# Kernel tuning notes

Measured on AMD Instinct MI355X. Metric: run time of the kernel, lower is better.

The kernel has to match this reference:

```python
import jax, jax.numpy as jnp
import numpy as np

D_MODEL, D_HEAD, N_HEAD, PERIOD = 1024, 64, 16, 30
B, T1, T2 = 2, 2048, 2048


def setup_inputs() -> dict:
    key = jax.random.key(0)
    ks = jax.random.split(key, 7)
    s_in = 1.0 / np.sqrt(D_MODEL)
    s_out = 1.0 / np.sqrt(N_HEAD * D_HEAD)
    return {
        "x": jax.random.normal(ks[0], (B, T1, D_MODEL), dtype=jnp.float32),
        "context": jax.random.normal(ks[1], (B, T2, D_MODEL), dtype=jnp.float32),
        "Wq": jax.random.uniform(ks[2], (N_HEAD * D_HEAD, D_MODEL), jnp.float32, -s_in, s_in),
        "Wk": jax.random.uniform(ks[3], (N_HEAD * D_HEAD, D_MODEL), jnp.float32, -s_in, s_in),
        "Wv": jax.random.uniform(ks[4], (N_HEAD * D_HEAD, D_MODEL), jnp.float32, -s_in, s_in),
        "Wo": jax.random.uniform(ks[5], (D_MODEL, N_HEAD * D_HEAD), jnp.float32, -s_out, s_out),
        "bo": jax.random.uniform(ks[6], (D_MODEL,), jnp.float32, -s_out, s_out),
    }


def reference(x, context, Wq, Wk, Wv, Wo, bo):
    Bx, T1x, _ = x.shape
    T2x = context.shape[1]
    scale = 1.0 / np.sqrt(D_HEAD).astype(np.float32)
    # projections (torch Linear: y = x @ W^T)
    q = (x @ Wq.T).reshape(Bx, T1x, N_HEAD, D_HEAD)
    k = (context @ Wk.T).reshape(Bx, T2x, N_HEAD, D_HEAD)
    v = (context @ Wv.T).reshape(Bx, T2x, N_HEAD, D_HEAD)
    # attention scores [B, H, T1, T2]
    scores = jnp.einsum('bihd,bjhd->bhij', q, k) * scale
    # ALiBi-style periodic distance bias
    dist = jnp.abs(jnp.arange(T1x)[:, None] - jnp.arange(T2x)[None, :])  # [T1,T2]
    bias = -(dist // PERIOD).astype(jnp.float32)                          # [T1,T2]
    head_scale = jnp.power(2.0, -jnp.arange(1, N_HEAD + 1, dtype=jnp.float32))
    biased = scores + bias[None, None, :, :] * head_scale[None, :, None, None]
    attn = jax.nn.softmax(biased, axis=-1)
    out = jnp.einsum('bhij,bjhd->bihd', attn, v).reshape(Bx, T1x, N_HEAD * D_HEAD)
    # output projection; dropout is identity in eval mode
    return out @ Wo.T + bo
```

## Files before the change

### kernel.cpp

```cpp
#include <hip/hip_runtime.h>
#include <hip/hip_fp16.h>

typedef _Float16 f16;
typedef __attribute__((ext_vector_type(8))) _Float16 f16x8;
typedef __attribute__((ext_vector_type(4))) _Float16 f16x4;
typedef __attribute__((ext_vector_type(2))) __fp16 fp16x2;
typedef __attribute__((ext_vector_type(4))) float f32x4;
typedef __attribute__((ext_vector_type(16))) float f32x16;

#define DM 1024
#define NH 16
#define DH 64
#define TT 2048
#define LOG2E 1.4426950408889634f
#define QSCALE 0.18033688f

__device__ __forceinline__ void gl16(const void* g, void* l) {
  __builtin_amdgcn_global_load_lds((const __attribute__((address_space(1))) void*)g,
                                   (__attribute__((address_space(3))) void*)l, 16, 0, 0);
}

__global__ __launch_bounds__(256) void cvt_all(const float* __restrict__ x, const float* __restrict__ cx,
                                               const float* __restrict__ wq, const float* __restrict__ wk,
                                               const float* __restrict__ wv, const float* __restrict__ wo,
                                               f16* __restrict__ xb, f16* __restrict__ cb,
                                               f16* __restrict__ wqb, f16* __restrict__ wkb,
                                               f16* __restrict__ wvb, f16* __restrict__ wob) {
  int idx = blockIdx.x * 256 + threadIdx.x;
  int stride = gridDim.x * 256;
  for (int i = idx; i < 3145728; i += stride) {
    const float* src; f16* dst; int off; float s = 1.0f;
    if (i < 2097152) {
      if (i < 1048576) { src = x; dst = xb; off = i; }
      else { src = cx; dst = cb; off = i - 1048576; }
    } else {
      int j = i - 2097152;
      int wsel = j >> 18;
      off = j & 262143;
      if (wsel == 0) { src = wq; dst = wqb; s = QSCALE; }
      else if (wsel == 1) { src = wk; dst = wkb; }
      else if (wsel == 2) { src = wv; dst = wvb; }
      else { src = wo; dst = wob; }
    }
    float4 v = reinterpret_cast<const float4*>(src)[off];
    f16x4 o = { (f16)(v.x * s), (f16)(v.y * s), (f16)(v.z * s), (f16)(v.w * s) };
    reinterpret_cast<f16x4*>(dst)[off] = o;
  }
}

__global__ __launch_bounds__(256) void fbgen(f16* __restrict__ FB) {
  int i = blockIdx.x;
  int j0 = threadIdx.x * 8;
  f16x8 v;
#pragma unroll
  for (int e = 0; e < 8; e++) {
    int d = i - (j0 + e); d = (d < 0) ? -d : d;
    v[e] = (f16)(d / 30);
  }
  *reinterpret_cast<f16x8*>(&FB[(size_t)i * TT + j0]) = v;
}

__device__ __forceinline__ void gemm_mainloop(const f16* __restrict__ A, const f16* __restrict__ W,
                                              int bm, int bn, f16 (*As)[4096], f16 (*Bs)[4096],
                                              f32x4 (&acc)[4][4]) {
  int t = threadIdx.x;
  int w = t >> 6;
  int lane = t & 63, lr = lane & 15, g = lane >> 4;
  int wr = w >> 1, wc = w & 1;
  int scol = ((t & 3) ^ ((t >> 3) & 3)) * 8;
  const f16* a0 = A + (size_t)(bm + (t >> 2)) * DM + scol;
  const f16* b0 = W + (size_t)(bn + (t >> 2)) * DM + scol;
  int wo = w * 512;
  int szg = ((lr >> 1) & 3) << 4;

  auto STG = [&](int bufi, int kt) {
    gl16(a0 + kt, As[bufi] + wo);
    gl16(a0 + kt + (size_t)64 * DM, As[bufi] + 2048 + wo);
    gl16(b0 + kt, Bs[bufi] + wo);
    gl16(b0 + kt + (size_t)64 * DM, Bs[bufi] + 2048 + wo);
  };

  STG(0, 0);
  __syncthreads();
  int buf = 0;
  for (int kt = 0; kt < DM; kt += 32) {
    if (kt + 32 < DM) STG(buf ^ 1, kt + 32);
    const char* Ab = (const char*)As[buf];
    const char* Bb = (const char*)Bs[buf];
    f16x8 af[4], bf[4];
#pragma unroll
    for (int mi = 0; mi < 4; mi++) {
      int row = wr * 64 + mi * 16 + lr;
      af[mi] = *reinterpret_cast<const f16x8*>(Ab + row * 64 + ((g << 4) ^ szg));
    }
#pragma unroll
    for (int ni = 0; ni < 4; ni++) {
      int row = wc * 64 + ni * 16 + lr;
      bf[ni] = *reinterpret_cast<const f16x8*>(Bb + row * 64 + ((g << 4) ^ szg));
    }
    __builtin_amdgcn_s_setprio(1);
#pragma unroll
    for (int mi = 0; mi < 4; mi++)
#pragma unroll
      for (int ni = 0; ni < 4; ni++)
        acc[mi][ni] = __builtin_amdgcn_mfma_f32_16x16x32_f16(af[mi], bf[ni], acc[mi][ni], 0, 0, 0);
    __builtin_amdgcn_s_setprio(0);
    __syncthreads();
    buf ^= 1;
  }
}

__global__ __launch_bounds__(256) void qkv_gemm(const f16* __restrict__ xb, const f16* __restrict__ cb,
                                                const f16* __restrict__ wq, const f16* __restrict__ wk,
                                                const f16* __restrict__ wv,
                                                f16* __restrict__ Qo, f16* __restrict__ Ko,
                                                f16* __restrict__ Vt) {
  __shared__ f16 As[2][4096];
  __shared__ f16 Bs[2][4096];
  int gid = blockIdx.x >> 8;
  int bid = blockIdx.x & 255;
  int bm = (bid >> 3) * 128, bn = (bid & 7) * 128;
  const f16* A = (gid == 0) ? xb : cb;
  const f16* W = (gid == 0) ? wq : ((gid == 1) ? wk : wv);
  f32x4 acc[4][4] = {};
  gemm_mainloop(A, W, bm, bn, As, Bs, acc);

  int t = threadIdx.x, w = t >> 6, lane = t & 63, lr = lane & 15, g = lane >> 4;
  int wr = w >> 1, wc = w & 1;
  if (gid < 2) {
    f16* out = (gid == 0) ? Qo : Ko;
#pragma unroll
    for (int mi = 0; mi < 4; mi++) {
      int m0 = bm + wr * 64 + mi * 16 + 4 * g;
      int b = m0 >> 11, i0 = m0 & 2047;
#pragma unroll
      for (int ni = 0; ni < 4; ni++) {
        int n = bn + wc * 64 + ni * 16 + lr;
        int h = n >> 6, d = n & 63;
        size_t base = (((size_t)(b * NH + h)) * TT + i0) * DH + d;
#pragma unroll
        for (int r = 0; r < 4; r++)
          out[base + (size_t)r * DH] = (f16)acc[mi][ni][r];
      }
    }
  } else {
#pragma unroll
    for (int mi = 0; mi < 4; mi++) {
      int m0 = bm + wr * 64 + mi * 16 + 4 * g;
      int b = m0 >> 11, j0 = m0 & 2047;
#pragma unroll
      for (int ni = 0; ni < 4; ni++) {
        int n = bn + wc * 64 + ni * 16 + lr;
        int h = n >> 6, d = n & 63;
        f16x4 pk = { (f16)acc[mi][ni][0], (f16)acc[mi][ni][1],
                     (f16)acc[mi][ni][2], (f16)acc[mi][ni][3] };
        *reinterpret_cast<f16x4*>(&Vt[(((size_t)(b * NH + h)) * DH + d) * TT + j0]) = pk;
      }
    }
  }
}

__global__ __launch_bounds__(256) void out_gemm(const f16* __restrict__ Ob, const f16* __restrict__ wo,
                                                const float* __restrict__ bo, float* __restrict__ Y) {
  __shared__ f16 As[2][4096];
  __shared__ f16 Bs[2][4096];
  int bid = blockIdx.x;
  int bm = (bid >> 3) * 128, bn = (bid & 7) * 128;
  f32x4 acc[4][4] = {};
  gemm_mainloop(Ob, wo, bm, bn, As, Bs, acc);
  int t = threadIdx.x, w = t >> 6, lane = t & 63, lr = lane & 15, g = lane >> 4;
  int wr = w >> 1, wc = w & 1;
#pragma unroll
  for (int mi = 0; mi < 4; mi++) {
    int m0 = bm + wr * 64 + mi * 16 + 4 * g;
#pragma unroll
    for (int ni = 0; ni < 4; ni++) {
      int n = bn + wc * 64 + ni * 16 + lr;
      float bias = bo[n];
#pragma unroll
      for (int r = 0; r < 4; r++)
        Y[(size_t)(m0 + r) * DM + n] = acc[mi][ni][r] + bias;
    }
  }
}

__global__ __launch_bounds__(128, 2) void attn_kernel(const f16* __restrict__ Q, const f16* __restrict__ K,
                                                      const f16* __restrict__ V, const f16* __restrict__ FB,
                                                      f16* __restrict__ O) {
  __shared__ f16 KV[2][8192];
  int o = blockIdx.x;
  int x = o & 7, idx = o >> 3;
  int bh = 4 * x + (idx >> 5), qt = idx & 31;
  int h = bh & 15, b = bh >> 4;
  int t = threadIdx.x, w = t >> 6, lane = t & 63;
  int col = lane & 31, hi = lane >> 5;
  int qi = qt * 64 + w * 32 + col;

  const f16* qp = Q + ((size_t)bh * TT + qi) * DH + hi * 8;
  f16x8 qf[4];
  qf[0] = *reinterpret_cast<const f16x8*>(qp);
  qf[1] = *reinterpret_cast<const f16x8*>(qp + 16);
  qf[2] = *reinterpret_cast<const f16x8*>(qp + 32);
  qf[3] = *reinterpret_cast<const f16x8*>(qp + 48);

  const float nc2 = -exp2f(-(float)(h + 1)) * LOG2E;
  const f16* fbrow = FB + (size_t)qi * TT + hi * 8;

  f32x4 rsv = { 0.f, 0.f, 0.f, 0.f };
  f32x16 oacc[2] = {};

  int r = lane >> 3, gcol = lane & 7;
  const f16 *kp[4], *vp[4];
#pragma unroll
  for (int c = 0; c < 4; c++) {
    int dg = gcol ^ r ^ (3 * (c >> 1));
    int J = 32 * w + 16 * (c >> 1) + 8 * (r >> 2) + 4 * (c & 1) + (r & 3);
    kp[c] = K + ((size_t)bh * TT + J) * DH + dg * 8;
    int dv = 32 * w + 8 * c + r;
    vp[c] = V + ((size_t)bh * DH + dv) * TT + dg * 8;
  }
  f16* ldsK = KV[0] + w * 2048;

  auto STG = [&](int bufi, int kvo) {
    f16* base = KV[bufi] + w * 2048;
#pragma unroll
    for (int c = 0; c < 4; c++) {
      gl16(kp[c] + (size_t)kvo * DH, base + c * 512);
      gl16(vp[c] + kvo, base + 4096 + c * 512);
    }
  };

  int rbase = col * 128;
  int fr = (lane & 7) ^ (3 * ((lane >> 4) & 1));
  int gsw[4];
#pragma unroll
  for (int s = 0; s < 4; s++) gsw[s] = ((2 * s + hi) ^ fr) << 4;

  STG(0, 0);
  __syncthreads();
  int buf = 0;

  for (int kv0 = 0; kv0 < TT; kv0 += 64) {
    if (kv0 + 64 < TT) STG(buf ^ 1, kv0 + 64);
    f16x8 fbv[4];
    fbv[0] = *reinterpret_cast<const f16x8*>(fbrow + kv0);
    fbv[1] = *reinterpret_cast<const f16x8*>(fbrow + kv0 + 16);
    fbv[2] = *reinterpret_cast<const f16x8*>(fbrow + kv0 + 32);
    fbv[3] = *reinterpret_cast<const f16x8*>(fbrow + kv0 + 48);

    const char* Kb = (const char*)KV[buf];
    const char* Vb = Kb + 8192;

    f32x16 sj[2] = {};
    __builtin_amdgcn_s_setprio(1);
#pragma unroll
    for (int s = 0; s < 4; s++) {
      f16x8 ka = *reinterpret_cast<const f16x8*>(Kb + rbase + gsw[s]);
      f16x8 kb = *reinterpret_cast<const f16x8*>(Kb + 4096 + rbase + gsw[s]);
      sj[0] = __builtin_amdgcn_mfma_f32_32x32x16_f16(ka, qf[s], sj[0], 0, 0, 0);
      sj[1] = __builtin_amdgcn_mfma_f32_32x32x16_f16(kb, qf[s], sj[1], 0, 0, 0);
    }
    __builtin_amdgcn_s_setprio(0);

    f16x8 pb[4];
#pragma unroll
    for (int s = 0; s < 4; s++) {
      const int jb = s >> 1, ro = 8 * (s & 1);
      float p[8];
#pragma unroll
      for (int e = 0; e < 8; e++) {
        float sx = fmaf((float)fbv[s][e], nc2, sj[jb][ro + e]);
        p[e] = __builtin_amdgcn_exp2f(sx);
      }
      f32x4 pl = { p[0], p[1], p[2], p[3] };
      f32x4 ph = { p[4], p[5], p[6], p[7] };
      rsv += pl + ph;
      union { f16x8 v; fp16x2 hh[4]; } pu;
      pu.hh[0] = __builtin_amdgcn_cvt_pkrtz(p[0], p[1]);
      pu.hh[1] = __builtin_amdgcn_cvt_pkrtz(p[2], p[3]);
      pu.hh[2] = __builtin_amdgcn_cvt_pkrtz(p[4], p[5]);
      pu.hh[3] = __builtin_amdgcn_cvt_pkrtz(p[6], p[7]);
      pb[s] = pu.v;
    }

    __builtin_amdgcn_s_setprio(1);
#pragma unroll
    for (int s = 0; s < 4; s++) {
      f16x8 va0 = *reinterpret_cast<const f16x8*>(Vb + rbase + gsw[s]);
      f16x8 va1 = *reinterpret_cast<const f16x8*>(Vb + 4096 + rbase + gsw[s]);
      oacc[0] = __builtin_amdgcn_mfma_f32_32x32x16_f16(va0, pb[s], oacc[0], 0, 0, 0);
      oacc[1] = __builtin_amdgcn_mfma_f32_32x32x16_f16(va1, pb[s], oacc[1], 0, 0, 0);
    }
    __builtin_amdgcn_s_setprio(0);
    __syncthreads();
    buf ^= 1;
  }

  float lsum = (rsv[0] + rsv[1]) + (rsv[2] + rsv[3]);
  lsum += __shfl_xor(lsum, 32, 64);
  float inv = __builtin_amdgcn_rcpf(lsum);

  size_t ob = ((size_t)b * TT + qi) * DM + h * DH + 4 * hi;
#pragma unroll
  for (int db = 0; db < 2; db++)
#pragma unroll
    for (int k = 0; k < 4; k++) {
      f16x4 o4 = { (f16)(oacc[db][4 * k] * inv),     (f16)(oacc[db][4 * k + 1] * inv),
                   (f16)(oacc[db][4 * k + 2] * inv), (f16)(oacc[db][4 * k + 3] * inv) };
      *reinterpret_cast<f16x4*>(&O[ob + 32 * db + 8 * k]) = o4;
    }
}

extern "C" void kernel_launch(void* const* d_in, const int* in_sizes, int n_in,
                              void* d_out, int out_size, void* d_ws, size_t ws_size,
                              hipStream_t stream) {
  const float* x  = (const float*)d_in[0];
  const float* cx = (const float*)d_in[1];
  const float* Wq = (const float*)d_in[2];
  const float* Wk = (const float*)d_in[3];
  const float* Wv = (const float*)d_in[4];
  const float* Wo = (const float*)d_in[5];
  const float* bo = (const float*)d_in[6];
  float* Y = (float*)d_out;

  const size_t NTOK = (size_t)2 * TT;
  f16* p = (f16*)d_ws;
  f16* xb  = p; p += NTOK * DM;
  f16* cb  = p; p += NTOK * DM;
  f16* wqb = p; p += (size_t)DM * DM;
  f16* wkb = p; p += (size_t)DM * DM;
  f16* wvb = p; p += (size_t)DM * DM;
  f16* wob = p; p += (size_t)DM * DM;
  f16* Qb  = p; p += NTOK * DM;
  f16* Kb  = p; p += NTOK * DM;
  f16* Vtb = p; p += NTOK * DM;
  f16* Ob  = p; p += NTOK * DM;
  f16* FBt = xb;

  cvt_all<<<2048, 256, 0, stream>>>(x, cx, Wq, Wk, Wv, Wo, xb, cb, wqb, wkb, wvb, wob);
  qkv_gemm<<<768, 256, 0, stream>>>(xb, cb, wqb, wkb, wvb, Qb, Kb, Vtb);
  fbgen<<<TT, 256, 0, stream>>>(FBt);
  attn_kernel<<<1024, 128, 0, stream>>>(Qb, Kb, Vtb, FBt, Ob);
  out_gemm<<<256, 256, 0, stream>>>(Ob, wob, bo, Y);
}
```

Before: 135.6 us.

## Software-pipeline attention QK^T with softmax/PV across tiles and fuse bias generation

The attention loop is restructured so the QK^T MFMAs and V fragment loads for the next KV tile are issued before the exp/PV work of the current tile. Two register sets of scores, bias and V fragments alternate, with the loop unrolled by two. Separately, the periodic-distance bias table is now built inside the conversion kernel and stored in its own workspace region instead of reusing xb, which removes one kernel launch. The trade-off is higher register pressure, which may reduce occupancy, and a larger workspace.

After: 133.1 us. No clear change (-1.8%).

```diff
diff --git a/kernel.cpp b/kernel.cpp
--- a/kernel.cpp
+++ b/kernel.cpp
@@ -25,10 +25,24 @@
                                                const float* __restrict__ wv, const float* __restrict__ wo,
                                                f16* __restrict__ xb, f16* __restrict__ cb,
                                                f16* __restrict__ wqb, f16* __restrict__ wkb,
-                                               f16* __restrict__ wvb, f16* __restrict__ wob) {
+                                               f16* __restrict__ wvb, f16* __restrict__ wob,
+                                               f16* __restrict__ FB) {
   int idx = blockIdx.x * 256 + threadIdx.x;
   int stride = gridDim.x * 256;
-  for (int i = idx; i < 3145728; i += stride) {
+  for (int i = idx; i < 3670016; i += stride) {
+    if (i >= 3145728) {
+      int c = i - 3145728;
+      int row = c >> 8;
+      int j0 = (c & 255) << 3;
+      f16x8 v;
+#pragma unroll
+      for (int e = 0; e < 8; e++) {
+        int d = row - (j0 + e); d = (d < 0) ? -d : d;
+        v[e] = (f16)(d / 30);
+      }
+      *reinterpret_cast<f16x8*>(&FB[(size_t)row * TT + j0]) = v;
+      continue;
+    }
     const float* src; f16* dst; int off; float s = 1.0f;
     if (i < 2097152) {
       if (i < 1048576) { src = x; dst = xb; off = i; }
@@ -46,18 +60,6 @@
     f16x4 o = { (f16)(v.x * s), (f16)(v.y * s), (f16)(v.z * s), (f16)(v.w * s) };
     reinterpret_cast<f16x4*>(dst)[off] = o;
   }
-}
-
-__global__ __launch_bounds__(256) void fbgen(f16* __restrict__ FB) {
-  int i = blockIdx.x;
-  int j0 = threadIdx.x * 8;
-  f16x8 v;
-#pragma unroll
-  for (int e = 0; e < 8; e++) {
-    int d = i - (j0 + e); d = (d < 0) ? -d : d;
-    v[e] = (f16)(d / 30);
-  }
-  *reinterpret_cast<f16x8*>(&FB[(size_t)i * TT + j0]) = v;
 }
 
 __device__ __forceinline__ void gemm_mainloop(const f16* __restrict__ A, const f16* __restrict__ W,
@@ -219,7 +221,6 @@
     int dv = 32 * w + 8 * c + r;
     vp[c] = V + ((size_t)bh * DH + dv) * TT + dg * 8;
   }
-  f16* ldsK = KV[0] + w * 2048;
 
   auto STG = [&](int bufi, int kvo) {
     f16* base = KV[bufi] + w * 2048;
@@ -236,40 +237,45 @@
 #pragma unroll
   for (int s = 0; s < 4; s++) gsw[s] = ((2 * s + hi) ^ fr) << 4;
 
-  STG(0, 0);
-  __syncthreads();
-  int buf = 0;
-
-  for (int kv0 = 0; kv0 < TT; kv0 += 64) {
-    if (kv0 + 64 < TT) STG(buf ^ 1, kv0 + 64);
-    f16x8 fbv[4];
+  f32x16 sA0, sA1, sB0, sB1;
+  f16x8 fA[4], fB[4], vA8[8], vB8[8];
+
+  auto QKT = [&](int kv0, int bufi, f32x16& sj0, f32x16& sj1,
+                 f16x8 (&fbv)[4], f16x8 (&vv)[8]) {
     fbv[0] = *reinterpret_cast<const f16x8*>(fbrow + kv0);
     fbv[1] = *reinterpret_cast<const f16x8*>(fbrow + kv0 + 16);
     fbv[2] = *reinterpret_cast<const f16x8*>(fbrow + kv0 + 32);
     fbv[3] = *reinterpret_cast<const f16x8*>(fbrow + kv0 + 48);
-
-    const char* Kb = (const char*)KV[buf];
+    const char* Kb = (const char*)KV[bufi];
     const char* Vb = Kb + 8192;
-
-    f32x16 sj[2] = {};
+    f32x16 z0 = {}, z1 = {};
     __builtin_amdgcn_s_setprio(1);
 #pragma unroll
     for (int s = 0; s < 4; s++) {
       f16x8 ka = *reinterpret_cast<const f16x8*>(Kb + rbase + gsw[s]);
       f16x8 kb = *reinterpret_cast<const f16x8*>(Kb + 4096 + rbase + gsw[s]);
-      sj[0] = __builtin_amdgcn_mfma_f32_32x32x16_f16(ka, qf[s], sj[0], 0, 0, 0);
-      sj[1] = __builtin_amdgcn_mfma_f32_32x32x16_f16(kb, qf[s], sj[1], 0, 0, 0);
+      z0 = __builtin_amdgcn_mfma_f32_32x32x16_f16(ka, qf[s], z0, 0, 0, 0);
+      z1 = __builtin_amdgcn_mfma_f32_32x32x16_f16(kb, qf[s], z1, 0, 0, 0);
     }
     __builtin_amdgcn_s_setprio(0);
-
+    sj0 = z0; sj1 = z1;
+#pragma unroll
+    for (int s = 0; s < 4; s++) {
+      vv[2 * s]     = *reinterpret_cast<const f16x8*>(Vb + rbase + gsw[s]);
+      vv[2 * s + 1] = *reinterpret_cast<const f16x8*>(Vb + 4096 + rbase + gsw[s]);
+    }
+  };
+
+  auto FIN = [&](f32x16& sj0, f32x16& sj1, f16x8 (&fbv)[4], f16x8 (&vv)[8]) {
     f16x8 pb[4];
 #pragma unroll
     for (int s = 0; s < 4; s++) {
-      const int jb = s >> 1, ro = 8 * (s & 1);
+      const int ro = 8 * (s & 1);
       float p[8];
 #pragma unroll
       for (int e = 0; e < 8; e++) {
-        float sx = fmaf((float)fbv[s][e], nc2, sj[jb][ro + e]);
+        float sval = (s < 2) ? sj0[ro + e] : sj1[ro + e];
+        float sx = fmaf((float)fbv[s][e], nc2, sval);
         p[e] = __builtin_amdgcn_exp2f(sx);
       }
       f32x4 pl = { p[0], p[1], p[2], p[3] };
@@ -282,19 +288,35 @@
       pu.hh[3] = __builtin_amdgcn_cvt_pkrtz(p[6], p[7]);
       pb[s] = pu.v;
     }
-
     __builtin_amdgcn_s_setprio(1);
 #pragma unroll
     for (int s = 0; s < 4; s++) {
-      f16x8 va0 = *reinterpret_cast<const f16x8*>(Vb + rbase + gsw[s]);
-      f16x8 va1 = *reinterpret_cast<const f16x8*>(Vb + 4096 + rbase + gsw[s]);
-      oacc[0] = __builtin_amdgcn_mfma_f32_32x32x16_f16(va0, pb[s], oacc[0], 0, 0, 0);
-      oacc[1] = __builtin_amdgcn_mfma_f32_32x32x16_f16(va1, pb[s], oacc[1], 0, 0, 0);
+      oacc[0] = __builtin_amdgcn_mfma_f32_32x32x16_f16(vv[2 * s],     pb[s], oacc[0], 0, 0, 0);
+      oacc[1] = __builtin_amdgcn_mfma_f32_32x32x16_f16(vv[2 * s + 1], pb[s], oacc[1], 0, 0, 0);
     }
     __builtin_amdgcn_s_setprio(0);
+  };
+
+  STG(0, 0);
+  __syncthreads();
+  STG(1, 64);
+  QKT(0, 0, sA0, sA1, fA, vA8);
+
+  for (int tp = 0; tp < 15; tp++) {
+    int kv0 = 64 + tp * 128;
     __syncthreads();
-    buf ^= 1;
-  }
+    STG(0, kv0 + 64);
+    QKT(kv0, 1, sB0, sB1, fB, vB8);
+    FIN(sA0, sA1, fA, vA8);
+    __syncthreads();
+    STG(1, kv0 + 128);
+    QKT(kv0 + 64, 0, sA0, sA1, fA, vA8);
+    FIN(sB0, sB1, fB, vB8);
+  }
+  __syncthreads();
+  QKT(TT - 64, 1, sB0, sB1, fB, vB8);
+  FIN(sA0, sA1, fA, vA8);
+  FIN(sB0, sB1, fB, vB8);
 
   float lsum = (rsv[0] + rsv[1]) + (rsv[2] + rsv[3]);
   lsum += __shfl_xor(lsum, 32, 64);
@@ -335,11 +357,10 @@
   f16* Kb  = p; p += NTOK * DM;
   f16* Vtb = p; p += NTOK * DM;
   f16* Ob  = p; p += NTOK * DM;
-  f16* FBt = xb;
-
-  cvt_all<<<2048, 256, 0, stream>>>(x, cx, Wq, Wk, Wv, Wo, xb, cb, wqb, wkb, wvb, wob);
+  f16* FBt = p;
+
+  cvt_all<<<2048, 256, 0, stream>>>(x, cx, Wq, Wk, Wv, Wo, xb, cb, wqb, wkb, wvb, wob, FBt);
   qkv_gemm<<<768, 256, 0, stream>>>(xb, cb, wqb, wkb, wvb, Qb, Kb, Vtb);
-  fbgen<<<TT, 256, 0, stream>>>(FBt);
   attn_kernel<<<1024, 128, 0, stream>>>(Qb, Kb, Vtb, FBt, Ob);
   out_gemm<<<256, 256, 0, stream>>>(Ob, wob, bo, Y);
 }
```

## Split KV tile across waves in attention and fold bias-table generation into conversion

Applied to the files above, without the earlier changes.

Attention now has each wave compute both 32-row query blocks against its own half of the 64-key tile, rather than each wave owning one query block and the full tile. This halves the per-wave K/V LDS reads per MFMA and requires a cross-wave reduction of the partial outputs and row sums through shared memory at the end. The bias-table generation moves into the conversion kernel, which removes one launch. The table now lives in its own workspace region instead of aliasing xb, so it needs a larger workspace.

New measurement: 134.0 us. About the same (-1.2%).

```diff
diff --git a/kernel.cpp b/kernel.cpp
--- a/kernel.cpp
+++ b/kernel.cpp
@@ -25,10 +25,24 @@
                                                const float* __restrict__ wv, const float* __restrict__ wo,
                                                f16* __restrict__ xb, f16* __restrict__ cb,
                                                f16* __restrict__ wqb, f16* __restrict__ wkb,
-                                               f16* __restrict__ wvb, f16* __restrict__ wob) {
+                                               f16* __restrict__ wvb, f16* __restrict__ wob,
+                                               f16* __restrict__ FB) {
   int idx = blockIdx.x * 256 + threadIdx.x;
   int stride = gridDim.x * 256;
-  for (int i = idx; i < 3145728; i += stride) {
+  for (int i = idx; i < 3670016; i += stride) {
+    if (i >= 3145728) {
+      int c = i - 3145728;
+      int row = c >> 8;
+      int j0 = (c & 255) << 3;
+      f16x8 v;
+#pragma unroll
+      for (int e = 0; e < 8; e++) {
+        int d = row - (j0 + e); d = (d < 0) ? -d : d;
+        v[e] = (f16)(d / 30);
+      }
+      *reinterpret_cast<f16x8*>(&FB[(size_t)row * TT + j0]) = v;
+      continue;
+    }
     const float* src; f16* dst; int off; float s = 1.0f;
     if (i < 2097152) {
       if (i < 1048576) { src = x; dst = xb; off = i; }
@@ -46,18 +60,6 @@
     f16x4 o = { (f16)(v.x * s), (f16)(v.y * s), (f16)(v.z * s), (f16)(v.w * s) };
     reinterpret_cast<f16x4*>(dst)[off] = o;
   }
-}
-
-__global__ __launch_bounds__(256) void fbgen(f16* __restrict__ FB) {
-  int i = blockIdx.x;
-  int j0 = threadIdx.x * 8;
-  f16x8 v;
-#pragma unroll
-  for (int e = 0; e < 8; e++) {
-    int d = i - (j0 + e); d = (d < 0) ? -d : d;
-    v[e] = (f16)(d / 30);
-  }
-  *reinterpret_cast<f16x8*>(&FB[(size_t)i * TT + j0]) = v;
 }
 
 __device__ __forceinline__ void gemm_mainloop(const f16* __restrict__ A, const f16* __restrict__ W,
@@ -194,47 +196,50 @@
   int h = bh & 15, b = bh >> 4;
   int t = threadIdx.x, w = t >> 6, lane = t & 63;
   int col = lane & 31, hi = lane >> 5;
-  int qi = qt * 64 + w * 32 + col;
-
-  const f16* qp = Q + ((size_t)bh * TT + qi) * DH + hi * 8;
-  f16x8 qf[4];
-  qf[0] = *reinterpret_cast<const f16x8*>(qp);
-  qf[1] = *reinterpret_cast<const f16x8*>(qp + 16);
-  qf[2] = *reinterpret_cast<const f16x8*>(qp + 32);
-  qf[3] = *reinterpret_cast<const f16x8*>(qp + 48);
+  int qi0 = qt * 64 + col;
+
+  const f16* qp0 = Q + ((size_t)bh * TT + qi0) * DH + hi * 8;
+  f16x8 qf0[4], qf1[4];
+#pragma unroll
+  for (int s = 0; s < 4; s++) {
+    qf0[s] = *reinterpret_cast<const f16x8*>(qp0 + 16 * s);
+    qf1[s] = *reinterpret_cast<const f16x8*>(qp0 + 32 * DH + 16 * s);
+  }
 
   const float nc2 = -exp2f(-(float)(h + 1)) * LOG2E;
-  const f16* fbrow = FB + (size_t)qi * TT + hi * 8;
-
-  f32x4 rsv = { 0.f, 0.f, 0.f, 0.f };
-  f32x16 oacc[2] = {};
-
-  int r = lane >> 3, gcol = lane & 7;
+  const f16* fbrow0 = FB + (size_t)qi0 * TT + 32 * w + 8 * hi;
+  const f16* fbrow1 = fbrow0 + (size_t)32 * TT;
+
+  float rsv0 = 0.f, rsv1 = 0.f;
+  f32x16 o00 = {}, o01 = {}, o10 = {}, o11 = {};
+
+  int r8 = lane >> 3, gcol = lane & 7;
   const f16 *kp[4], *vp[4];
 #pragma unroll
-  for (int c = 0; c < 4; c++) {
-    int dg = gcol ^ r ^ (3 * (c >> 1));
-    int J = 32 * w + 16 * (c >> 1) + 8 * (r >> 2) + 4 * (c & 1) + (r & 3);
-    kp[c] = K + ((size_t)bh * TT + J) * DH + dg * 8;
-    int dv = 32 * w + 8 * c + r;
-    vp[c] = V + ((size_t)bh * DH + dv) * TT + dg * 8;
-  }
-  f16* ldsK = KV[0] + w * 2048;
-
+  for (int cc = 0; cc < 4; cc++) {
+    int dg = gcol ^ r8 ^ (3 * (cc >> 1));
+    int J = 32 * w + 16 * (cc >> 1) + 8 * (r8 >> 2) + 4 * (cc & 1) + (r8 & 3);
+    kp[cc] = K + ((size_t)bh * TT + J) * DH + dg * 8;
+    int dv = 32 * w + 8 * cc + r8;
+    vp[cc] = V + ((size_t)bh * DH + dv) * TT + dg * 8;
+  }
   auto STG = [&](int bufi, int kvo) {
     f16* base = KV[bufi] + w * 2048;
 #pragma unroll
-    for (int c = 0; c < 4; c++) {
-      gl16(kp[c] + (size_t)kvo * DH, base + c * 512);
-      gl16(vp[c] + kvo, base + 4096 + c * 512);
+    for (int cc = 0; cc < 4; cc++) {
+      gl16(kp[cc] + (size_t)kvo * DH, base + cc * 512);
+      gl16(vp[cc] + kvo, base + 4096 + cc * 512);
     }
   };
 
-  int rbase = col * 128;
-  int fr = (lane & 7) ^ (3 * ((lane >> 4) & 1));
-  int gsw[4];
-#pragma unroll
-  for (int s = 0; s < 4; s++) gsw[s] = ((2 * s + hi) ^ fr) << 4;
+  int fcol = (col & 7) ^ (3 * ((col >> 4) & 1));
+  int kbase = (32 * w + col) * 128;
+  int vbase = 8192 + col * 128;
+  int ksw[4], vsw[2];
+#pragma unroll
+  for (int s = 0; s < 4; s++) ksw[s] = ((2 * s + hi) ^ fcol) << 4;
+#pragma unroll
+  for (int s2 = 0; s2 < 2; s2++) vsw[s2] = ((4 * w + 2 * s2 + hi) ^ fcol) << 4;
 
   STG(0, 0);
   __syncthreads();
@@ -242,73 +247,103 @@
 
   for (int kv0 = 0; kv0 < TT; kv0 += 64) {
     if (kv0 + 64 < TT) STG(buf ^ 1, kv0 + 64);
-    f16x8 fbv[4];
-    fbv[0] = *reinterpret_cast<const f16x8*>(fbrow + kv0);
-    fbv[1] = *reinterpret_cast<const f16x8*>(fbrow + kv0 + 16);
-    fbv[2] = *reinterpret_cast<const f16x8*>(fbrow + kv0 + 32);
-    fbv[3] = *reinterpret_cast<const f16x8*>(fbrow + kv0 + 48);
+    f16x8 fb00 = *reinterpret_cast<const f16x8*>(fbrow0 + kv0);
+    f16x8 fb01 = *reinterpret_cast<const f16x8*>(fbrow0 + kv0 + 16);
+    f16x8 fb10 = *reinterpret_cast<const f16x8*>(fbrow1 + kv0);
+    f16x8 fb11 = *reinterpret_cast<const f16x8*>(fbrow1 + kv0 + 16);
 
     const char* Kb = (const char*)KV[buf];
-    const char* Vb = Kb + 8192;
-
-    f32x16 sj[2] = {};
+
+    f32x16 s0 = {}, s1 = {};
     __builtin_amdgcn_s_setprio(1);
 #pragma unroll
     for (int s = 0; s < 4; s++) {
-      f16x8 ka = *reinterpret_cast<const f16x8*>(Kb + rbase + gsw[s]);
-      f16x8 kb = *reinterpret_cast<const f16x8*>(Kb + 4096 + rbase + gsw[s]);
-      sj[0] = __builtin_amdgcn_mfma_f32_32x32x16_f16(ka, qf[s], sj[0], 0, 0, 0);
-      sj[1] = __builtin_amdgcn_mfma_f32_32x32x16_f16(kb, qf[s], sj[1], 0, 0, 0);
+      f16x8 ka = *reinterpret_cast<const f16x8*>(Kb + kbase + ksw[s]);
+      s0 = __builtin_amdgcn_mfma_f32_32x32x16_f16(ka, qf0[s], s0, 0, 0, 0);
+      s1 = __builtin_amdgcn_mfma_f32_32x32x16_f16(ka, qf1[s], s1, 0, 0, 0);
     }
     __builtin_amdgcn_s_setprio(0);
 
-    f16x8 pb[4];
-#pragma unroll
-    for (int s = 0; s < 4; s++) {
-      const int jb = s >> 1, ro = 8 * (s & 1);
-      float p[8];
+    f16x8 pb0[2], pb1[2];
+#pragma unroll
+    for (int s2 = 0; s2 < 2; s2++) {
+      float p0[8], p1[8];
 #pragma unroll
       for (int e = 0; e < 8; e++) {
-        float sx = fmaf((float)fbv[s][e], nc2, sj[jb][ro + e]);
-        p[e] = __builtin_amdgcn_exp2f(sx);
-      }
-      f32x4 pl = { p[0], p[1], p[2], p[3] };
-      f32x4 ph = { p[4], p[5], p[6], p[7] };
-      rsv += pl + ph;
-      union { f16x8 v; fp16x2 hh[4]; } pu;
-      pu.hh[0] = __builtin_amdgcn_cvt_pkrtz(p[0], p[1]);
-      pu.hh[1] = __builtin_amdgcn_cvt_pkrtz(p[2], p[3]);
-      pu.hh[2] = __builtin_amdgcn_cvt_pkrtz(p[4], p[5]);
-      pu.hh[3] = __builtin_amdgcn_cvt_pkrtz(p[6], p[7]);
-      pb[s] = pu.v;
+        float f0 = (float)((s2 == 0) ? fb00[e] : fb01[e]);
+        float f1 = (float)((s2 == 0) ? fb10[e] : fb11[e]);
+        p0[e] = __builtin_amdgcn_exp2f(fmaf(f0, nc2, s0[8 * s2 + e]));
+        p1[e] = __builtin_amdgcn_exp2f(fmaf(f1, nc2, s1[8 * s2 + e]));
+      }
+#pragma unroll
+      for (int e = 0; e < 8; e++) { rsv0 += p0[e]; rsv1 += p1[e]; }
+      union { f16x8 v; fp16x2 hh[4]; } u0, u1;
+#pragma unroll
+      for (int q2 = 0; q2 < 4; q2++) {
+        u0.hh[q2] = __builtin_amdgcn_cvt_pkrtz(p0[2 * q2], p0[2 * q2 + 1]);
+        u1.hh[q2] = __builtin_amdgcn_cvt_pkrtz(p1[2 * q2], p1[2 * q2 + 1]);
+      }
+      pb0[s2] = u0.v; pb1[s2] = u1.v;
     }
 
     __builtin_amdgcn_s_setprio(1);
 #pragma unroll
-    for (int s = 0; s < 4; s++) {
-      f16x8 va0 = *reinterpret_cast<const f16x8*>(Vb + rbase + gsw[s]);
-      f16x8 va1 = *reinterpret_cast<const f16x8*>(Vb + 4096 + rbase + gsw[s]);
-      oacc[0] = __builtin_amdgcn_mfma_f32_32x32x16_f16(va0, pb[s], oacc[0], 0, 0, 0);
-      oacc[1] = __builtin_amdgcn_mfma_f32_32x32x16_f16(va1, pb[s], oacc[1], 0, 0, 0);
+    for (int s2 = 0; s2 < 2; s2++) {
+      f16x8 va0 = *reinterpret_cast<const f16x8*>(Kb + vbase + vsw[s2]);
+      f16x8 va1 = *reinterpret_cast<const f16x8*>(Kb + vbase + 4096 + vsw[s2]);
+      o00 = __builtin_amdgcn_mfma_f32_32x32x16_f16(va0, pb0[s2], o00, 0, 0, 0);
+      o01 = __builtin_amdgcn_mfma_f32_32x32x16_f16(va1, pb0[s2], o01, 0, 0, 0);
+      o10 = __builtin_amdgcn_mfma_f32_32x32x16_f16(va0, pb1[s2], o10, 0, 0, 0);
+      o11 = __builtin_amdgcn_mfma_f32_32x32x16_f16(va1, pb1[s2], o11, 0, 0, 0);
     }
     __builtin_amdgcn_s_setprio(0);
     __syncthreads();
     buf ^= 1;
   }
 
-  float lsum = (rsv[0] + rsv[1]) + (rsv[2] + rsv[3]);
-  lsum += __shfl_xor(lsum, 32, 64);
-  float inv = __builtin_amdgcn_rcpf(lsum);
-
-  size_t ob = ((size_t)b * TT + qi) * DM + h * DH + 4 * hi;
-#pragma unroll
-  for (int db = 0; db < 2; db++)
-#pragma unroll
-    for (int k = 0; k < 4; k++) {
-      f16x4 o4 = { (f16)(oacc[db][4 * k] * inv),     (f16)(oacc[db][4 * k + 1] * inv),
-                   (f16)(oacc[db][4 * k + 2] * inv), (f16)(oacc[db][4 * k + 3] * inv) };
-      *reinterpret_cast<f16x4*>(&O[ob + 32 * db + 8 * k]) = o4;
-    }
+  rsv0 += __shfl_xor(rsv0, 32, 64);
+  rsv1 += __shfl_xor(rsv1, 32, 64);
+  float* red = (float*)KV;
+  if (lane < 32) {
+    red[4096 + (w * 2 + 0) * 32 + col] = rsv0;
+    red[4096 + (w * 2 + 1) * 32 + col] = rsv1;
+  }
+  if (w == 1) {
+    const f32x16* oa[4] = { &o00, &o01, &o10, &o11 };
+#pragma unroll
+    for (int q2 = 0; q2 < 4; q2++)
+#pragma unroll
+      for (int r = 0; r < 16; r++) {
+        int rA = (r & 3) + 8 * (r >> 2) + 4 * hi;
+        red[(q2 * 32 + rA) * 32 + col] = (*oa[q2])[r];
+      }
+  }
+  __syncthreads();
+  if (w == 0) {
+    float ls0 = red[4096 + col] + red[4096 + 64 + col];
+    float ls1 = red[4096 + 32 + col] + red[4096 + 96 + col];
+    float inv0 = __builtin_amdgcn_rcpf(ls0);
+    float inv1 = __builtin_amdgcn_rcpf(ls1);
+    const f32x16* oa[4] = { &o00, &o01, &o10, &o11 };
+#pragma unroll
+    for (int q2 = 0; q2 < 4; q2++) {
+      int qb = q2 >> 1, db = q2 & 1;
+      float inv = qb ? inv1 : inv0;
+      size_t ob = ((size_t)b * TT + qt * 64 + 32 * qb + col) * DM + h * DH + 32 * db + 4 * hi;
+#pragma unroll
+      for (int a = 0; a < 4; a++) {
+        f16x4 o4;
+#pragma unroll
+        for (int e = 0; e < 4; e++) {
+          int r = 4 * a + e;
+          int rA = (r & 3) + 8 * (r >> 2) + 4 * hi;
+          float v = (*oa[q2])[r] + red[(q2 * 32 + rA) * 32 + col];
+          o4[e] = (f16)(v * inv);
+        }
+        *reinterpret_cast<f16x4*>(&O[ob + 8 * a]) = o4;
+      }
+    }
+  }
 }
 
 extern "C" void kernel_launch(void* const* d_in, const int* in_sizes, int n_in,
@@ -335,11 +370,10 @@
   f16* Kb  = p; p += NTOK * DM;
   f16* Vtb = p; p += NTOK * DM;
   f16* Ob  = p; p += NTOK * DM;
-  f16* FBt = xb;
-
-  cvt_all<<<2048, 256, 0, stream>>>(x, cx, Wq, Wk, Wv, Wo, xb, cb, wqb, wkb, wvb, wob);
+  f16* FBt = p;
+
+  cvt_all<<<2048, 256, 0, stream>>>(x, cx, Wq, Wk, Wv, Wo, xb, cb, wqb, wkb, wvb, wob, FBt);
   qkv_gemm<<<768, 256, 0, stream>>>(xb, cb, wqb, wkb, wvb, Qb, Kb, Vtb);
-  fbgen<<<TT, 256, 0, stream>>>(FBt);
   attn_kernel<<<1024, 128, 0, stream>>>(Qb, Kb, Vtb, FBt, Ob);
   out_gemm<<<256, 256, 0, stream>>>(Ob, wob, bo, Y);
 }
```

## Restructure attention into single-wave blocks with manual pipelining and fragment-ordered bias

Applied to the files above, without the earlier changes.

The attention kernel now runs one 64-thread wave per block, each handling 32 queries over 32-key tiles. The loop is manually unrolled into two LDS buffers, with sched_barriers and explicit vmcnt waits so loads overlap with compute and the block-wide __syncthreads disappears. The distance-bias table is precomputed inside the conversion kernel in the exact per-lane fragment order, so the separate fbgen launch is removed and bias loads are contiguous. The risks are lower MFMA work per LDS load, that the hand-counted waitcnt is fragile, and the extra workspace needed for the bias table.

Result: slower. 144.1 us (+6.3%).

```diff
diff --git a/kernel.cpp b/kernel.cpp
--- a/kernel.cpp
+++ b/kernel.cpp
@@ -20,15 +20,32 @@
                                    (__attribute__((address_space(3))) void*)l, 16, 0, 0);
 }
 
+#define SB0 __builtin_amdgcn_sched_barrier(0)
+
 __global__ __launch_bounds__(256) void cvt_all(const float* __restrict__ x, const float* __restrict__ cx,
                                                const float* __restrict__ wq, const float* __restrict__ wk,
                                                const float* __restrict__ wv, const float* __restrict__ wo,
                                                f16* __restrict__ xb, f16* __restrict__ cb,
                                                f16* __restrict__ wqb, f16* __restrict__ wkb,
-                                               f16* __restrict__ wvb, f16* __restrict__ wob) {
+                                               f16* __restrict__ wvb, f16* __restrict__ wob,
+                                               f16* __restrict__ FBf) {
   int idx = blockIdx.x * 256 + threadIdx.x;
   int stride = gridDim.x * 256;
-  for (int i = idx; i < 3145728; i += stride) {
+  for (int i = idx; i < 3670016; i += stride) {
+    if (i >= 3145728) {
+      int c = i - 3145728;
+      int half = c & 1, lane = (c >> 1) & 63, kvt = (c >> 7) & 63, qt = c >> 13;
+      int qi = qt * 32 + (lane & 31);
+      int jb = kvt * 32 + 16 * half + 8 * (lane >> 5);
+      f16x8 v;
+#pragma unroll
+      for (int e = 0; e < 8; e++) {
+        int d = qi - (jb + e); d = (d < 0) ? -d : d;
+        v[e] = (f16)(d / 30);
+      }
+      reinterpret_cast<f16x8*>(FBf)[c] = v;
+      continue;
+    }
     const float* src; f16* dst; int off; float s = 1.0f;
     if (i < 2097152) {
       if (i < 1048576) { src = x; dst = xb; off = i; }
@@ -46,18 +63,6 @@
     f16x4 o = { (f16)(v.x * s), (f16)(v.y * s), (f16)(v.z * s), (f16)(v.w * s) };
     reinterpret_cast<f16x4*>(dst)[off] = o;
   }
-}
-
-__global__ __launch_bounds__(256) void fbgen(f16* __restrict__ FB) {
-  int i = blockIdx.x;
-  int j0 = threadIdx.x * 8;
-  f16x8 v;
-#pragma unroll
-  for (int e = 0; e < 8; e++) {
-    int d = i - (j0 + e); d = (d < 0) ? -d : d;
-    v[e] = (f16)(d / 30);
-  }
-  *reinterpret_cast<f16x8*>(&FB[(size_t)i * TT + j0]) = v;
 }
 
 __device__ __forceinline__ void gemm_mainloop(const f16* __restrict__ A, const f16* __restrict__ W,
@@ -184,116 +189,129 @@
   }
 }
 
-__global__ __launch_bounds__(128, 2) void attn_kernel(const f16* __restrict__ Q, const f16* __restrict__ K,
-                                                      const f16* __restrict__ V, const f16* __restrict__ FB,
-                                                      f16* __restrict__ O) {
-  __shared__ f16 KV[2][8192];
+__global__ __launch_bounds__(64, 2) void attn_kernel(const f16* __restrict__ Q, const f16* __restrict__ K,
+                                                     const f16* __restrict__ V, const f16* __restrict__ FBf,
+                                                     f16* __restrict__ O) {
+  __shared__ f16 KV[2][4096];
   int o = blockIdx.x;
-  int x = o & 7, idx = o >> 3;
-  int bh = 4 * x + (idx >> 5), qt = idx & 31;
+  int xcd = o & 7, idx = o >> 3;
+  int bh = 4 * xcd + (idx >> 6), qt = idx & 63;
   int h = bh & 15, b = bh >> 4;
-  int t = threadIdx.x, w = t >> 6, lane = t & 63;
-  int col = lane & 31, hi = lane >> 5;
-  int qi = qt * 64 + w * 32 + col;
+  int l = threadIdx.x;
+  int col = l & 31, hi = l >> 5;
+  int qi = qt * 32 + col;
 
   const f16* qp = Q + ((size_t)bh * TT + qi) * DH + hi * 8;
   f16x8 qf[4];
-  qf[0] = *reinterpret_cast<const f16x8*>(qp);
-  qf[1] = *reinterpret_cast<const f16x8*>(qp + 16);
-  qf[2] = *reinterpret_cast<const f16x8*>(qp + 32);
-  qf[3] = *reinterpret_cast<const f16x8*>(qp + 48);
+#pragma unroll
+  for (int s = 0; s < 4; s++) qf[s] = *reinterpret_cast<const f16x8*>(qp + 16 * s);
 
   const float nc2 = -exp2f(-(float)(h + 1)) * LOG2E;
-  const f16* fbrow = FB + (size_t)qi * TT + hi * 8;
+  const f16x8* fbp = reinterpret_cast<const f16x8*>(FBf) + ((size_t)qt << 13) + (l << 1);
 
   f32x4 rsv = { 0.f, 0.f, 0.f, 0.f };
-  f32x16 oacc[2] = {};
-
-  int r = lane >> 3, gcol = lane & 7;
-  const f16 *kp[4], *vp[4];
+  f32x16 oacc0 = {}, oacc1 = {};
+
+  int r8 = l >> 3, G = l & 7;
+  const f16 *kps[4], *vps[4];
 #pragma unroll
   for (int c = 0; c < 4; c++) {
-    int dg = gcol ^ r ^ (3 * (c >> 1));
-    int J = 32 * w + 16 * (c >> 1) + 8 * (r >> 2) + 4 * (c & 1) + (r & 3);
-    kp[c] = K + ((size_t)bh * TT + J) * DH + dg * 8;
-    int dv = 32 * w + 8 * c + r;
-    vp[c] = V + ((size_t)bh * DH + dv) * TT + dg * 8;
-  }
-  f16* ldsK = KV[0] + w * 2048;
-
-  auto STG = [&](int bufi, int kvo) {
-    f16* base = KV[bufi] + w * 2048;
-#pragma unroll
-    for (int c = 0; c < 4; c++) {
-      gl16(kp[c] + (size_t)kvo * DH, base + c * 512);
-      gl16(vp[c] + kvo, base + 4096 + c * 512);
-    }
+    int rho = c * 8 + r8;
+    int g0k = G ^ (rho & 7);
+    int J = (rho & 19) | ((rho & 4) << 1) | ((rho & 8) >> 1);
+    kps[c] = K + ((size_t)bh * TT + J) * DH + g0k * 8;
+    int pi = c * 8 + r8;
+    int g0v = G ^ (pi & 7);
+    int dv = 2 * pi + (g0v >> 2), jg = g0v & 3;
+    vps[c] = V + ((size_t)bh * DH + dv) * TT + jg * 8;
+  }
+
+  auto STG = [&](int bufi, int kv0) {
+    f16* base = KV[bufi];
+#pragma unroll
+    for (int c = 0; c < 4; c++) gl16(kps[c] + (size_t)kv0 * DH, base + c * 512);
+#pragma unroll
+    for (int c = 0; c < 4; c++) gl16(vps[c] + kv0, base + 2048 + c * 512);
   };
 
-  int rbase = col * 128;
-  int fr = (lane & 7) ^ (3 * ((lane >> 4) & 1));
-  int gsw[4];
-#pragma unroll
-  for (int s = 0; s < 4; s++) gsw[s] = ((2 * s + hi) ^ fr) << 4;
+  int kbase = col * 128;
+  int ksw[4];
+#pragma unroll
+  for (int s = 0; s < 4; s++) ksw[s] = ((2 * s + hi) ^ (col & 7)) << 4;
+  int vbyte[2][2];
+#pragma unroll
+  for (int db = 0; db < 2; db++)
+#pragma unroll
+    for (int s2 = 0; s2 < 2; s2++) {
+      int pi = 16 * db + (col >> 1);
+      int gl = (col & 1) * 4 + 2 * s2 + hi;
+      vbyte[db][s2] = 4096 + pi * 128 + ((gl ^ (pi & 7)) << 4);
+    }
+
+  auto CMP = [&](int bufi, f16x8 fb0, f16x8 fb1) {
+    const char* Kb = (const char*)KV[bufi];
+    f32x16 S = {};
+    __builtin_amdgcn_s_setprio(1);
+#pragma unroll
+    for (int s = 0; s < 4; s++) {
+      f16x8 ka = *reinterpret_cast<const f16x8*>(Kb + kbase + ksw[s]);
+      S = __builtin_amdgcn_mfma_f32_32x32x16_f16(ka, qf[s], S, 0, 0, 0);
+    }
+    __builtin_amdgcn_s_setprio(0);
+    float p[16];
+#pragma unroll
+    for (int r = 0; r < 16; r++) {
+      float fbf = (float)((r < 8) ? fb0[r] : fb1[r - 8]);
+      p[r] = __builtin_amdgcn_exp2f(fmaf(fbf, nc2, S[r]));
+    }
+#pragma unroll
+    for (int r = 0; r < 4; r++) {
+      f32x4 pv = { p[4 * r], p[4 * r + 1], p[4 * r + 2], p[4 * r + 3] };
+      rsv += pv;
+    }
+    f16x8 pb[2];
+#pragma unroll
+    for (int s2 = 0; s2 < 2; s2++) {
+      union { f16x8 v; fp16x2 hh[4]; } pu;
+#pragma unroll
+      for (int q2 = 0; q2 < 4; q2++)
+        pu.hh[q2] = __builtin_amdgcn_cvt_pkrtz(p[8 * s2 + 2 * q2], p[8 * s2 + 2 * q2 + 1]);
+      pb[s2] = pu.v;
+    }
+    __builtin_amdgcn_s_setprio(1);
+#pragma unroll
+    for (int s2 = 0; s2 < 2; s2++) {
+      f16x8 va0 = *reinterpret_cast<const f16x8*>(Kb + vbyte[0][s2]);
+      f16x8 va1 = *reinterpret_cast<const f16x8*>(Kb + vbyte[1][s2]);
+      oacc0 = __builtin_amdgcn_mfma_f32_32x32x16_f16(va0, pb[s2], oacc0, 0, 0, 0);
+      oacc1 = __builtin_amdgcn_mfma_f32_32x32x16_f16(va1, pb[s2], oacc1, 0, 0, 0);
+    }
+    __builtin_amdgcn_s_setprio(0);
+  };
 
   STG(0, 0);
-  __syncthreads();
-  int buf = 0;
-
-  for (int kv0 = 0; kv0 < TT; kv0 += 64) {
-    if (kv0 + 64 < TT) STG(buf ^ 1, kv0 + 64);
-    f16x8 fbv[4];
-    fbv[0] = *reinterpret_cast<const f16x8*>(fbrow + kv0);
-    fbv[1] = *reinterpret_cast<const f16x8*>(fbrow + kv0 + 16);
-    fbv[2] = *reinterpret_cast<const f16x8*>(fbrow + kv0 + 32);
-    fbv[3] = *reinterpret_cast<const f16x8*>(fbrow + kv0 + 48);
-
-    const char* Kb = (const char*)KV[buf];
-    const char* Vb = Kb + 8192;
-
-    f32x16 sj[2] = {};
-    __builtin_amdgcn_s_setprio(1);
-#pragma unroll
-    for (int s = 0; s < 4; s++) {
-      f16x8 ka = *reinterpret_cast<const f16x8*>(Kb + rbase + gsw[s]);
-      f16x8 kb = *reinterpret_cast<const f16x8*>(Kb + 4096 + rbase + gsw[s]);
-      sj[0] = __builtin_amdgcn_mfma_f32_32x32x16_f16(ka, qf[s], sj[0], 0, 0, 0);
-      sj[1] = __builtin_amdgcn_mfma_f32_32x32x16_f16(kb, qf[s], sj[1], 0, 0, 0);
-    }
-    __builtin_amdgcn_s_setprio(0);
-
-    f16x8 pb[4];
-#pragma unroll
-    for (int s = 0; s < 4; s++) {
-      const int jb = s >> 1, ro = 8 * (s & 1);
-      float p[8];
-#pragma unroll
-      for (int e = 0; e < 8; e++) {
-        float sx = fmaf((float)fbv[s][e], nc2, sj[jb][ro + e]);
-        p[e] = __builtin_amdgcn_exp2f(sx);
-      }
-      f32x4 pl = { p[0], p[1], p[2], p[3] };
-      f32x4 ph = { p[4], p[5], p[6], p[7] };
-      rsv += pl + ph;
-      union { f16x8 v; fp16x2 hh[4]; } pu;
-      pu.hh[0] = __builtin_amdgcn_cvt_pkrtz(p[0], p[1]);
-      pu.hh[1] = __builtin_amdgcn_cvt_pkrtz(p[2], p[3]);
-      pu.hh[2] = __builtin_amdgcn_cvt_pkrtz(p[4], p[5]);
-      pu.hh[3] = __builtin_amdgcn_cvt_pkrtz(p[6], p[7]);
-      pb[s] = pu.v;
-    }
-
-    __builtin_amdgcn_s_setprio(1);
-#pragma unroll
-    for (int s = 0; s < 4; s++) {
-      f16x8 va0 = *reinterpret_cast<const f16x8*>(Vb + rbase + gsw[s]);
-      f16x8 va1 = *reinterpret_cast<const f16x8*>(Vb + 4096 + rbase + gsw[s]);
-      oacc[0] = __builtin_amdgcn_mfma_f32_32x32x16_f16(va0, pb[s], oacc[0], 0, 0, 0);
-      oacc[1] = __builtin_amdgcn_mfma_f32_32x32x16_f16(va1, pb[s], oacc[1], 0, 0, 0);
-    }
-    __builtin_amdgcn_s_setprio(0);
-    __syncthreads();
-    buf ^= 1;
+  f16x8 fA0 = fbp[0], fA1 = fbp[1];
+  f16x8 fB0, fB1;
+
+  for (int kvt = 0; kvt < 64; kvt += 2) {
+    SB0;
+    STG(1, (kvt + 1) << 5);
+    fB0 = fbp[(kvt + 1) * 128];
+    fB1 = fbp[(kvt + 1) * 128 + 1];
+    asm volatile("s_waitcnt vmcnt(10)" ::: "memory");
+    SB0;
+    CMP(0, fA0, fA1);
+    SB0;
+    if (kvt + 2 < 64) {
+      STG(0, (kvt + 2) << 5);
+      fA0 = fbp[(kvt + 2) * 128];
+      fA1 = fbp[(kvt + 2) * 128 + 1];
+      asm volatile("s_waitcnt vmcnt(10)" ::: "memory");
+    } else {
+      asm volatile("s_waitcnt vmcnt(0)" ::: "memory");
+    }
+    SB0;
+    CMP(1, fB0, fB1);
   }
 
   float lsum = (rsv[0] + rsv[1]) + (rsv[2] + rsv[3]);
@@ -301,13 +319,14 @@
   float inv = __builtin_amdgcn_rcpf(lsum);
 
   size_t ob = ((size_t)b * TT + qi) * DM + h * DH + 4 * hi;
+  const f32x16* oa[2] = { &oacc0, &oacc1 };
 #pragma unroll
   for (int db = 0; db < 2; db++)
 #pragma unroll
-    for (int k = 0; k < 4; k++) {
-      f16x4 o4 = { (f16)(oacc[db][4 * k] * inv),     (f16)(oacc[db][4 * k + 1] * inv),
-                   (f16)(oacc[db][4 * k + 2] * inv), (f16)(oacc[db][4 * k + 3] * inv) };
-      *reinterpret_cast<f16x4*>(&O[ob + 32 * db + 8 * k]) = o4;
+    for (int a = 0; a < 4; a++) {
+      f16x4 o4 = { (f16)((*oa[db])[4 * a] * inv),     (f16)((*oa[db])[4 * a + 1] * inv),
+                   (f16)((*oa[db])[4 * a + 2] * inv), (f16)((*oa[db])[4 * a + 3] * inv) };
+      *reinterpret_cast<f16x4*>(&O[ob + 32 * db + 8 * a]) = o4;
     }
 }
 
@@ -335,11 +354,10 @@
   f16* Kb  = p; p += NTOK * DM;
   f16* Vtb = p; p += NTOK * DM;
   f16* Ob  = p; p += NTOK * DM;
-  f16* FBt = xb;
-
-  cvt_all<<<2048, 256, 0, stream>>>(x, cx, Wq, Wk, Wv, Wo, xb, cb, wqb, wkb, wvb, wob);
+  f16* FBt = p;
+
+  cvt_all<<<2048, 256, 0, stream>>>(x, cx, Wq, Wk, Wv, Wo, xb, cb, wqb, wkb, wvb, wob, FBt);
   qkv_gemm<<<768, 256, 0, stream>>>(xb, cb, wqb, wkb, wvb, Qb, Kb, Vtb);
-  fbgen<<<TT, 256, 0, stream>>>(FBt);
-  attn_kernel<<<1024, 128, 0, stream>>>(Qb, Kb, Vtb, FBt, Ob);
+  attn_kernel<<<2048, 64, 0, stream>>>(Qb, Kb, Vtb, FBt, Ob);
   out_gemm<<<256, 256, 0, stream>>>(Ob, wob, bo, Y);
 }
```
